# Kernel optimization log

Hardware: AMD Instinct MI355X
Metric: run time of the kernel (lower is better)

The kernel has to match this reference:

```python
import jax, jax.numpy as jnp
import numpy as np

SCALE = 1.0 / np.sqrt(128.0)  # 1/sqrt(head_size)
NEG = -1000000000.0


def setup_inputs() -> dict:
    key = jax.random.key(0)
    k1, k2, k3, k4 = jax.random.split(key, 4)
    B, H, S, D = 2, 16, 2048, 128
    q = jax.random.normal(k1, (B, H, S, D), dtype=jnp.float32)
    k = jax.random.normal(k2, (B, H, S, D), dtype=jnp.float32)
    v = jax.random.normal(k3, (B, H, S, D), dtype=jnp.float32)
    mask = jax.random.randint(k4, (B, S), 0, 2, dtype=jnp.int32)
    return {"q": q, "k": k, "v": v, "mask": mask}


def reference(q, k, v, mask):
    # scores: [B, H, Sq, Sk]
    scores = jnp.einsum("bhqd,bhkd->bhqk", q, k) * SCALE
    m = mask[:, None, None, :]  # [B,1,1,Sk], broadcast over heads and queries
    scores = jnp.where(m == 0, NEG, scores)
    weights = jax.nn.softmax(scores, axis=-1)
    out = jnp.einsum("bhqk,bhkd->bhqd", weights, v)
    return out
```

## Files before the change

### kernel.cpp

```cpp
#include <hip/hip_runtime.h>
#include <hip/hip_bf16.h>

typedef __attribute__((ext_vector_type(8))) short short8;
typedef __attribute__((ext_vector_type(4))) short short4v;
typedef __attribute__((ext_vector_type(4))) float floatx4;

#define NB 2
#define NH 16
#define NBH 32
#define SS 2048
#define DD 128
#define BQ 128
#define BK 32
#define KTILES (SS / BK)
#define KPAIRS (KTILES / 2)
#define SCALE 0.08838834764831845f
#define LOG2E 1.4426950408889634f
#define MAXB 12.0f
#define MASKED_BIAS -100000.0f

#define WC_VM0 0x0F70
#define WC_LGKM0 0xC07F

__device__ __forceinline__ short f2bf(float f) {
  union { float f; unsigned u; } x; x.f = f;
  return (short)((x.u + 0x7FFFu + ((x.u >> 16) & 1u)) >> 16);
}

__device__ __forceinline__ void pack8(short8* dst, float a, float b, float c, float d,
                                      float e, float f, float g, float h) {
  union { __hip_bfloat162 h2[4]; short8 v; } u;
  u.h2[0] = __float22bfloat162_rn(make_float2(a, b));
  u.h2[1] = __float22bfloat162_rn(make_float2(c, d));
  u.h2[2] = __float22bfloat162_rn(make_float2(e, f));
  u.h2[3] = __float22bfloat162_rn(make_float2(g, h));
  *dst = u.v;
}

__device__ __forceinline__ void gload_lds16(const short* g, short* l) {
  __builtin_amdgcn_global_load_lds(
      (const __attribute__((address_space(1))) void*)(g),
      (__attribute__((address_space(3))) void*)(l), 16, 0, 0);
}

__global__ __launch_bounds__(256) void prep_kernel(const float* __restrict__ k,
                                                   const float* __restrict__ v,
                                                   short* __restrict__ kbf,
                                                   short* __restrict__ vtg) {
  __shared__ __align__(16) short Ts[DD * 64];
  const int kb = blockIdx.x, bh = blockIdx.y;
  const int tid = threadIdx.x;
  const size_t base = (size_t)bh * SS * DD + (size_t)(kb * 64) * DD;
  const float* kr = k + base;
  const float* vr = v + base;
  short* kw = kbf + base;

#pragma unroll
  for (int c = 0; c < 8; ++c) {
    int fi = c * 256 + tid;
    float4 a = ((const float4*)kr)[fi];
    short4v o;
    o[0] = f2bf(a.x); o[1] = f2bf(a.y); o[2] = f2bf(a.z); o[3] = f2bf(a.w);
    *(short4v*)(kw + (size_t)fi * 4) = o;
  }

  const int kg = tid & 15;
  const int dg0 = tid >> 4;
#pragma unroll
  for (int c = 0; c < 2; ++c) {
    int dg = dg0 + 16 * c;
    float rr[4][4];
#pragma unroll
    for (int r = 0; r < 4; ++r) {
      float4 a = ((const float4*)vr)[(kg * 4 + r) * 32 + dg];
      rr[r][0] = a.x; rr[r][1] = a.y; rr[r][2] = a.z; rr[r][3] = a.w;
    }
#pragma unroll
    for (int j = 0; j < 4; ++j) {
      int d = dg * 4 + j;
      short4v t;
      t[0] = f2bf(rr[0][j]); t[1] = f2bf(rr[1][j]);
      t[2] = f2bf(rr[2][j]); t[3] = f2bf(rr[3][j]);
      int si = d * 64 + (((kg * 8) ^ ((d & 15) << 3)) >> 1);
      *(short4v*)&Ts[si] = t;
    }
  }
  __syncthreads();

#pragma unroll
  for (int s = 0; s < 4; ++s) {
    int d = s * 32 + (tid >> 3);
    int c = tid & 7, kt2 = c >> 2, g = c & 3;
    int x = (d & 15) << 3;
    short4v lo = *(short4v*)&Ts[d * 64 + ((((kt2 * 8 + g) * 8) ^ x) >> 1)];
    short4v hi = *(short4v*)&Ts[d * 64 + ((((kt2 * 8 + g + 4) * 8) ^ x) >> 1)];
    short8 o;
#pragma unroll
    for (int r = 0; r < 4; ++r) { o[r] = lo[r]; o[4 + r] = hi[r]; }
    *(short8*)(vtg + ((size_t)(bh * DD + d)) * SS + (kb * 2 + kt2) * 32 + g * 8) = o;
  }
}

__global__ __launch_bounds__(256, 2) void fa_kernel(
    const float* __restrict__ q, const short* __restrict__ kbf,
    const short* __restrict__ vtg, const int* __restrict__ mask,
    float* __restrict__ out) {
  __shared__ __align__(16) short Ks[4][BK * DD];
  __shared__ __align__(16) short Vt[4][DD * BK];
  __shared__ float Bias[SS];

  const int tid = threadIdx.x;
  const int wave = tid >> 6;
  const int lane = tid & 63;
  const int l16 = lane & 15;
  const int quad = lane >> 4;

  const int lid = blockIdx.y * 16 + blockIdx.x;
  const int vid = (lid & 7) * 64 + (lid >> 3);
  const int bh = vid >> 4;
  const int q0 = (vid & 15) * BQ;
  const int b = bh >> 4;
  const int poff = ((bh >> 1) & 1) << 4;

  const size_t base = (size_t)bh * SS * DD;
  const float* qg = q + base;
  const short* kg = kbf + base;
  const short* vgb = vtg + (size_t)bh * DD * SS;
  const int* mg = mask + b * SS;
  const float c1 = SCALE * LOG2E, c2 = MAXB * LOG2E;

  short8 qf[2][4];
#pragma unroll
  for (int t = 0; t < 2; ++t) {
    const float* qp = qg + (size_t)(q0 + wave * 32 + t * 16 + l16) * DD;
#pragma unroll
    for (int dc = 0; dc < 4; ++dc) {
      float4 a = *(const float4*)(qp + dc * 32 + quad * 8);
      float4 bb = *(const float4*)(qp + dc * 32 + quad * 8 + 4);
      short8 tt;
      tt[0] = f2bf(a.x); tt[1] = f2bf(a.y); tt[2] = f2bf(a.z); tt[3] = f2bf(a.w);
      tt[4] = f2bf(bb.x); tt[5] = f2bf(bb.y); tt[6] = f2bf(bb.z); tt[7] = f2bf(bb.w);
      qf[t][dc] = tt;
    }
  }

  {
    int i0 = tid * 8;
    int4 m0 = *(const int4*)(mg + i0);
    int4 m1 = *(const int4*)(mg + i0 + 4);
    float4 f0, f1;
    f0.x = m0.x ? -c2 : MASKED_BIAS; f0.y = m0.y ? -c2 : MASKED_BIAS;
    f0.z = m0.z ? -c2 : MASKED_BIAS; f0.w = m0.w ? -c2 : MASKED_BIAS;
    f1.x = m1.x ? -c2 : MASKED_BIAS; f1.y = m1.y ? -c2 : MASKED_BIAS;
    f1.z = m1.z ? -c2 : MASKED_BIAS; f1.w = m1.w ? -c2 : MASKED_BIAS;
    *(float4*)&Bias[i0] = f0;
    *(float4*)&Bias[i0 + 4] = f1;
  }

  floatx4 Oacc[2][8];
#pragma unroll
  for (int t = 0; t < 2; ++t)
#pragma unroll
    for (int f = 0; f < 8; ++f) Oacc[t][f] = (floatx4){0.f, 0.f, 0.f, 0.f};
  float l_acc[2] = {0.f, 0.f};

  const short* kpg[2];
  const short* vpg[2];
  int kls[2], vls[2];
#pragma unroll
  for (int i = 0; i < 2; ++i) {
    int c = wave * 2 + i;
    int krow = c * 4 + (lane >> 4);
    kpg[i] = kg + (size_t)krow * DD + (((lane & 15) ^ (krow & 7)) * 8);
    int d = c * 16 + (lane >> 2);
    vpg[i] = vgb + (size_t)d * SS + (((lane & 3) ^ ((lane >> 3) & 3)) * 8);
    kls[i] = c * 512;
    vls[i] = c * 512;
  }

  int koff[2];
#pragma unroll
  for (int nt = 0; nt < 2; ++nt) koff[nt] = (nt * 16 + l16) * DD;
  const int ksw = l16 & 7;
  const int voff = l16 * 32 + ((quad ^ ((l16 >> 1) & 3)) * 8);

#pragma unroll
  for (int c = 0; c < 2; ++c) {
    const int ktp = 2 * poff + c;
    const size_t kadv = (size_t)ktp * (BK * DD);
    const int vadv = ktp * BK;
#pragma unroll
    for (int i = 0; i < 2; ++i) {
      gload_lds16(kpg[i] + kadv, &Ks[c][kls[i]]);
      gload_lds16(vpg[i] + vadv, &Vt[c][vls[i]]);
    }
  }
  __builtin_amdgcn_s_waitcnt(WC_LGKM0);

#pragma unroll 1
  for (int j = 0; j < KPAIRS; ++j) {
    __builtin_amdgcn_s_waitcnt(WC_VM0);
    __builtin_amdgcn_s_barrier();

    if (j + 1 < KPAIRS) {
      const int pp = (j + 1 + poff) & (KPAIRS - 1);
      const int tb = 2 * ((j + 1) & 1);
#pragma unroll
      for (int c = 0; c < 2; ++c) {
        const int ktn = 2 * pp + c;
        const size_t kadv = (size_t)ktn * (BK * DD);
        const int vadv = ktn * BK;
#pragma unroll
        for (int i = 0; i < 2; ++i) {
          gload_lds16(kpg[i] + kadv, &Ks[tb + c][kls[i]]);
          gload_lds16(vpg[i] + vadv, &Vt[tb + c][vls[i]]);
        }
      }
    }

    const int pp = (j + poff) & (KPAIRS - 1);
    const int ktA = 2 * pp, ktB = ktA + 1;
    const int tbA = 2 * (j & 1), tbB = tbA + 1;
    const short* ksA = &Ks[tbA][0];
    const short* ksB = &Ks[tbB][0];
    const short* vsA = &Vt[tbA][0];
    const short* vsB = &Vt[tbB][0];

    floatx4 sA[2][2], sB[2][2];
#pragma unroll
    for (int t = 0; t < 2; ++t)
#pragma unroll
      for (int nt = 0; nt < 2; ++nt) {
        sA[t][nt] = (floatx4){0.f, 0.f, 0.f, 0.f};
        sB[t][nt] = (floatx4){0.f, 0.f, 0.f, 0.f};
      }
    __builtin_amdgcn_s_setprio(1);
#pragma unroll
    for (int nt = 0; nt < 2; ++nt)
#pragma unroll
      for (int dc = 0; dc < 4; ++dc) {
        short8 kf = *(const short8*)(ksA + koff[nt] + (((dc * 4 + quad) ^ ksw) * 8));
        sA[0][nt] = __builtin_amdgcn_mfma_f32_16x16x32_bf16(kf, qf[0][dc], sA[0][nt], 0, 0, 0);
        sA[1][nt] = __builtin_amdgcn_mfma_f32_16x16x32_bf16(kf, qf[1][dc], sA[1][nt], 0, 0, 0);
      }
#pragma unroll
    for (int nt = 0; nt < 2; ++nt)
#pragma unroll
      for (int dc = 0; dc < 4; ++dc) {
        short8 kf = *(const short8*)(ksB + koff[nt] + (((dc * 4 + quad) ^ ksw) * 8));
        sB[0][nt] = __builtin_amdgcn_mfma_f32_16x16x32_bf16(kf, qf[0][dc], sB[0][nt], 0, 0, 0);
        sB[1][nt] = __builtin_amdgcn_mfma_f32_16x16x32_bf16(kf, qf[1][dc], sB[1][nt], 0, 0, 0);
      }
    __builtin_amdgcn_s_setprio(0);

    float4 bbA0 = *(const float4*)&Bias[ktA * 32 + quad * 4];
    float4 bbA1 = *(const float4*)&Bias[ktA * 32 + 16 + quad * 4];
    short8 pbA[2];
#pragma unroll
    for (int t = 0; t < 2; ++t) {
      float e0 = __builtin_amdgcn_exp2f(fmaf(sA[t][0][0], c1, bbA0.x));
      float e1 = __builtin_amdgcn_exp2f(fmaf(sA[t][0][1], c1, bbA0.y));
      float e2 = __builtin_amdgcn_exp2f(fmaf(sA[t][0][2], c1, bbA0.z));
      float e3 = __builtin_amdgcn_exp2f(fmaf(sA[t][0][3], c1, bbA0.w));
      float g0 = __builtin_amdgcn_exp2f(fmaf(sA[t][1][0], c1, bbA1.x));
      float g1 = __builtin_amdgcn_exp2f(fmaf(sA[t][1][1], c1, bbA1.y));
      float g2 = __builtin_amdgcn_exp2f(fmaf(sA[t][1][2], c1, bbA1.z));
      float g3 = __builtin_amdgcn_exp2f(fmaf(sA[t][1][3], c1, bbA1.w));
      l_acc[t] += ((e0 + e1) + (e2 + e3)) + ((g0 + g1) + (g2 + g3));
      pack8(&pbA[t], e0, e1, e2, e3, g0, g1, g2, g3);
    }

    __builtin_amdgcn_s_setprio(1);
#pragma unroll
    for (int f = 0; f < 8; ++f) {
      short8 vv = *(const short8*)(vsA + f * 512 + voff);
      Oacc[0][f] = __builtin_amdgcn_mfma_f32_16x16x32_bf16(vv, pbA[0], Oacc[0][f], 0, 0, 0);
      Oacc[1][f] = __builtin_amdgcn_mfma_f32_16x16x32_bf16(vv, pbA[1], Oacc[1][f], 0, 0, 0);
    }
    __builtin_amdgcn_s_setprio(0);

    float4 bbB0 = *(const float4*)&Bias[ktB * 32 + quad * 4];
    float4 bbB1 = *(const float4*)&Bias[ktB * 32 + 16 + quad * 4];
    short8 pbB[2];
#pragma unroll
    for (int t = 0; t < 2; ++t) {
      float e0 = __builtin_amdgcn_exp2f(fmaf(sB[t][0][0], c1, bbB0.x));
      float e1 = __builtin_amdgcn_exp2f(fmaf(sB[t][0][1], c1, bbB0.y));
      float e2 = __builtin_amdgcn_exp2f(fmaf(sB[t][0][2], c1, bbB0.z));
      float e3 = __builtin_amdgcn_exp2f(fmaf(sB[t][0][3], c1, bbB0.w));
      float g0 = __builtin_amdgcn_exp2f(fmaf(sB[t][1][0], c1, bbB1.x));
      float g1 = __builtin_amdgcn_exp2f(fmaf(sB[t][1][1], c1, bbB1.y));
      float g2 = __builtin_amdgcn_exp2f(fmaf(sB[t][1][2], c1, bbB1.z));
      float g3 = __builtin_amdgcn_exp2f(fmaf(sB[t][1][3], c1, bbB1.w));
      l_acc[t] += ((e0 + e1) + (e2 + e3)) + ((g0 + g1) + (g2 + g3));
      pack8(&pbB[t], e0, e1, e2, e3, g0, g1, g2, g3);
    }

    __builtin_amdgcn_s_setprio(1);
#pragma unroll
    for (int f = 0; f < 8; ++f) {
      short8 vv = *(const short8*)(vsB + f * 512 + voff);
      Oacc[0][f] = __builtin_amdgcn_mfma_f32_16x16x32_bf16(vv, pbB[0], Oacc[0][f], 0, 0, 0);
      Oacc[1][f] = __builtin_amdgcn_mfma_f32_16x16x32_bf16(vv, pbB[1], Oacc[1][f], 0, 0, 0);
    }
    __builtin_amdgcn_s_setprio(0);
  }

  float* og = out + base;
#pragma unroll
  for (int t = 0; t < 2; ++t) {
    float s = l_acc[t];
    s += __shfl_xor(s, 16);
    s += __shfl_xor(s, 32);
    float inv = 1.0f / s;
    float* orow = og + (size_t)(q0 + wave * 32 + t * 16 + l16) * DD + quad * 4;
#pragma unroll
    for (int f = 0; f < 8; ++f) {
      float4 w;
      w.x = Oacc[t][f][0] * inv;
      w.y = Oacc[t][f][1] * inv;
      w.z = Oacc[t][f][2] * inv;
      w.w = Oacc[t][f][3] * inv;
      *(float4*)(orow + f * 16) = w;
    }
  }
}

extern "C" void kernel_launch(void* const* d_in, const int* in_sizes, int n_in,
                              void* d_out, int out_size, void* d_ws, size_t ws_size,
                              hipStream_t stream) {
  const float* q = (const float*)d_in[0];
  const float* k = (const float*)d_in[1];
  const float* v = (const float*)d_in[2];
  const int* mask = (const int*)d_in[3];
  float* out = (float*)d_out;

  short* kbf = (short*)d_ws;
  short* vtg = kbf + (size_t)NBH * SS * DD;

  prep_kernel<<<dim3(SS / 64, NBH), dim3(256), 0, stream>>>(k, v, kbf, vtg);
  fa_kernel<<<dim3(SS / BQ, NBH), dim3(256), 0, stream>>>(q, kbf, vtg, mask, out);
}
```

Measured before the change: 201.2 us.

## Double query tile per block to 256 rows, four 16-row subtiles per wave

Raises the query block from 128 to 256 rows. Each wave now owns 64 query rows (four 16-row subtiles), so every K/V fragment read from LDS feeds twice as many MFMAs and each block streams K/V for twice as many queries. The grid shrinks to 256 blocks, and launch bounds drop to one block per SIMD to fit the doubled accumulator registers. The rotated K-tile start offset (poff) that spread blocks across the sequence is removed. Occupancy falls to one block per CU with 256 blocks on 256 CUs, which may hurt latency hiding.

```diff
diff --git a/kernel.cpp b/kernel.cpp
--- a/kernel.cpp
+++ b/kernel.cpp
@@ -10,7 +10,7 @@
 #define NBH 32
 #define SS 2048
 #define DD 128
-#define BQ 128
+#define BQ 256
 #define BK 32
 #define KTILES (SS / BK)
 #define KPAIRS (KTILES / 2)
@@ -101,7 +101,7 @@
   }
 }
 
-__global__ __launch_bounds__(256, 2) void fa_kernel(
+__global__ __launch_bounds__(256, 1) void fa_kernel(
     const float* __restrict__ q, const short* __restrict__ kbf,
     const short* __restrict__ vtg, const int* __restrict__ mask,
     float* __restrict__ out) {
@@ -115,12 +115,11 @@
   const int l16 = lane & 15;
   const int quad = lane >> 4;
 
-  const int lid = blockIdx.y * 16 + blockIdx.x;
-  const int vid = (lid & 7) * 64 + (lid >> 3);
-  const int bh = vid >> 4;
-  const int q0 = (vid & 15) * BQ;
+  const int lid = blockIdx.y * 8 + blockIdx.x;
+  const int vid = (lid & 7) * 32 + (lid >> 3);
+  const int bh = vid >> 3;
+  const int q0 = (vid & 7) * BQ;
   const int b = bh >> 4;
-  const int poff = ((bh >> 1) & 1) << 4;
 
   const size_t base = (size_t)bh * SS * DD;
   const float* qg = q + base;
@@ -129,10 +128,10 @@
   const int* mg = mask + b * SS;
   const float c1 = SCALE * LOG2E, c2 = MAXB * LOG2E;
 
-  short8 qf[2][4];
-#pragma unroll
-  for (int t = 0; t < 2; ++t) {
-    const float* qp = qg + (size_t)(q0 + wave * 32 + t * 16 + l16) * DD;
+  short8 qf[4][4];
+#pragma unroll
+  for (int t = 0; t < 4; ++t) {
+    const float* qp = qg + (size_t)(q0 + wave * 64 + t * 16 + l16) * DD;
 #pragma unroll
     for (int dc = 0; dc < 4; ++dc) {
       float4 a = *(const float4*)(qp + dc * 32 + quad * 8);
@@ -157,12 +156,12 @@
     *(float4*)&Bias[i0 + 4] = f1;
   }
 
-  floatx4 Oacc[2][8];
-#pragma unroll
-  for (int t = 0; t < 2; ++t)
+  floatx4 Oacc[4][8];
+#pragma unroll
+  for (int t = 0; t < 4; ++t)
 #pragma unroll
     for (int f = 0; f < 8; ++f) Oacc[t][f] = (floatx4){0.f, 0.f, 0.f, 0.f};
-  float l_acc[2] = {0.f, 0.f};
+  float l_acc[4] = {0.f, 0.f, 0.f, 0.f};
 
   const short* kpg[2];
   const short* vpg[2];
@@ -186,9 +185,8 @@
 
 #pragma unroll
   for (int c = 0; c < 2; ++c) {
-    const int ktp = 2 * poff + c;
-    const size_t kadv = (size_t)ktp * (BK * DD);
-    const int vadv = ktp * BK;
+    const size_t kadv = (size_t)c * (BK * DD);
+    const int vadv = c * BK;
 #pragma unroll
     for (int i = 0; i < 2; ++i) {
       gload_lds16(kpg[i] + kadv, &Ks[c][kls[i]]);
@@ -203,11 +201,10 @@
     __builtin_amdgcn_s_barrier();
 
     if (j + 1 < KPAIRS) {
-      const int pp = (j + 1 + poff) & (KPAIRS - 1);
       const int tb = 2 * ((j + 1) & 1);
 #pragma unroll
       for (int c = 0; c < 2; ++c) {
-        const int ktn = 2 * pp + c;
+        const int ktn = 2 * (j + 1) + c;
         const size_t kadv = (size_t)ktn * (BK * DD);
         const int vadv = ktn * BK;
 #pragma unroll
@@ -218,17 +215,16 @@
       }
     }
 
-    const int pp = (j + poff) & (KPAIRS - 1);
-    const int ktA = 2 * pp, ktB = ktA + 1;
+    const int ktA = 2 * j, ktB = ktA + 1;
     const int tbA = 2 * (j & 1), tbB = tbA + 1;
     const short* ksA = &Ks[tbA][0];
     const short* ksB = &Ks[tbB][0];
     const short* vsA = &Vt[tbA][0];
     const short* vsB = &Vt[tbB][0];
 
-    floatx4 sA[2][2], sB[2][2];
-#pragma unroll
-    for (int t = 0; t < 2; ++t)
+    floatx4 sA[4][2], sB[4][2];
+#pragma unroll
+    for (int t = 0; t < 4; ++t)
 #pragma unroll
       for (int nt = 0; nt < 2; ++nt) {
         sA[t][nt] = (floatx4){0.f, 0.f, 0.f, 0.f};
@@ -240,24 +236,26 @@
 #pragma unroll
       for (int dc = 0; dc < 4; ++dc) {
         short8 kf = *(const short8*)(ksA + koff[nt] + (((dc * 4 + quad) ^ ksw) * 8));
-        sA[0][nt] = __builtin_amdgcn_mfma_f32_16x16x32_bf16(kf, qf[0][dc], sA[0][nt], 0, 0, 0);
-        sA[1][nt] = __builtin_amdgcn_mfma_f32_16x16x32_bf16(kf, qf[1][dc], sA[1][nt], 0, 0, 0);
+#pragma unroll
+        for (int t = 0; t < 4; ++t)
+          sA[t][nt] = __builtin_amdgcn_mfma_f32_16x16x32_bf16(kf, qf[t][dc], sA[t][nt], 0, 0, 0);
       }
 #pragma unroll
     for (int nt = 0; nt < 2; ++nt)
 #pragma unroll
       for (int dc = 0; dc < 4; ++dc) {
         short8 kf = *(const short8*)(ksB + koff[nt] + (((dc * 4 + quad) ^ ksw) * 8));
-        sB[0][nt] = __builtin_amdgcn_mfma_f32_16x16x32_bf16(kf, qf[0][dc], sB[0][nt], 0, 0, 0);
-        sB[1][nt] = __builtin_amdgcn_mfma_f32_16x16x32_bf16(kf, qf[1][dc], sB[1][nt], 0, 0, 0);
+#pragma unroll
+        for (int t = 0; t < 4; ++t)
+          sB[t][nt] = __builtin_amdgcn_mfma_f32_16x16x32_bf16(kf, qf[t][dc], sB[t][nt], 0, 0, 0);
       }
     __builtin_amdgcn_s_setprio(0);
 
     float4 bbA0 = *(const float4*)&Bias[ktA * 32 + quad * 4];
     float4 bbA1 = *(const float4*)&Bias[ktA * 32 + 16 + quad * 4];
-    short8 pbA[2];
-#pragma unroll
-    for (int t = 0; t < 2; ++t) {
+    short8 pbA[4];
+#pragma unroll
+    for (int t = 0; t < 4; ++t) {
       float e0 = __builtin_amdgcn_exp2f(fmaf(sA[t][0][0], c1, bbA0.x));
       float e1 = __builtin_amdgcn_exp2f(fmaf(sA[t][0][1], c1, bbA0.y));
       float e2 = __builtin_amdgcn_exp2f(fmaf(sA[t][0][2], c1, bbA0.z));
@@ -274,16 +272,17 @@
 #pragma unroll
     for (int f = 0; f < 8; ++f) {
       short8 vv = *(const short8*)(vsA + f * 512 + voff);
-      Oacc[0][f] = __builtin_amdgcn_mfma_f32_16x16x32_bf16(vv, pbA[0], Oacc[0][f], 0, 0, 0);
-      Oacc[1][f] = __builtin_amdgcn_mfma_f32_16x16x32_bf16(vv, pbA[1], Oacc[1][f], 0, 0, 0);
+#pragma unroll
+      for (int t = 0; t < 4; ++t)
+        Oacc[t][f] = __builtin_amdgcn_mfma_f32_16x16x32_bf16(vv, pbA[t], Oacc[t][f], 0, 0, 0);
     }
     __builtin_amdgcn_s_setprio(0);
 
     float4 bbB0 = *(const float4*)&Bias[ktB * 32 + quad * 4];
     float4 bbB1 = *(const float4*)&Bias[ktB * 32 + 16 + quad * 4];
-    short8 pbB[2];
-#pragma unroll
-    for (int t = 0; t < 2; ++t) {
+    short8 pbB[4];
+#pragma unroll
+    for (int t = 0; t < 4; ++t) {
       float e0 = __builtin_amdgcn_exp2f(fmaf(sB[t][0][0], c1, bbB0.x));
       float e1 = __builtin_amdgcn_exp2f(fmaf(sB[t][0][1], c1, bbB0.y));
       float e2 = __builtin_amdgcn_exp2f(fmaf(sB[t][0][2], c1, bbB0.z));
@@ -300,20 +299,21 @@
 #pragma unroll
     for (int f = 0; f < 8; ++f) {
       short8 vv = *(const short8*)(vsB + f * 512 + voff);
-      Oacc[0][f] = __builtin_amdgcn_mfma_f32_16x16x32_bf16(vv, pbB[0], Oacc[0][f], 0, 0, 0);
-      Oacc[1][f] = __builtin_amdgcn_mfma_f32_16x16x32_bf16(vv, pbB[1], Oacc[1][f], 0, 0, 0);
+#pragma unroll
+      for (int t = 0; t < 4; ++t)
+        Oacc[t][f] = __builtin_amdgcn_mfma_f32_16x16x32_bf16(vv, pbB[t], Oacc[t][f], 0, 0, 0);
     }
     __builtin_amdgcn_s_setprio(0);
   }
 
   float* og = out + base;
 #pragma unroll
-  for (int t = 0; t < 2; ++t) {
+  for (int t = 0; t < 4; ++t) {
     float s = l_acc[t];
     s += __shfl_xor(s, 16);
     s += __shfl_xor(s, 32);
     float inv = 1.0f / s;
-    float* orow = og + (size_t)(q0 + wave * 32 + t * 16 + l16) * DD + quad * 4;
+    float* orow = og + (size_t)(q0 + wave * 64 + t * 16 + l16) * DD + quad * 4;
 #pragma unroll
     for (int f = 0; f < 8; ++f) {
       float4 w;
```

New measurement: 222.9 us. 1.11x slower.

## Fuse K/V bf16 conversion and V transpose into attention kernel, drop prep pass

Applied to the files above, without the earlier changes.

Removes the separate prep kernel that converted K to bf16 and wrote a transposed bf16 V to workspace. The attention kernel now loads fp32 K/V straight from global memory into registers, converts and transposes them while staging, and writes them into swizzled LDS buffers, with the loads for the next tile pair overlapped with the current tile's MFMA work. This saves a kernel launch and the workspace write/read round trip. In exchange each of the 16 query-block workgroups per head re-reads and re-converts K/V in fp32, roughly doubling global read bytes per block, and staging through registers adds pressure and VALU work.

```diff
diff --git a/kernel.cpp b/kernel.cpp
--- a/kernel.cpp
+++ b/kernel.cpp
@@ -5,8 +5,6 @@
 typedef __attribute__((ext_vector_type(4))) short short4v;
 typedef __attribute__((ext_vector_type(4))) float floatx4;
 
-#define NB 2
-#define NH 16
 #define NBH 32
 #define SS 2048
 #define DD 128
@@ -19,8 +17,9 @@
 #define MAXB 12.0f
 #define MASKED_BIAS -100000.0f
 
-#define WC_VM0 0x0F70
 #define WC_LGKM0 0xC07F
+
+typedef union { float4 v; float f[4]; } f4u;
 
 __device__ __forceinline__ short f2bf(float f) {
   union { float f; unsigned u; } x; x.f = f;
@@ -37,73 +36,9 @@
   *dst = u.v;
 }
 
-__device__ __forceinline__ void gload_lds16(const short* g, short* l) {
-  __builtin_amdgcn_global_load_lds(
-      (const __attribute__((address_space(1))) void*)(g),
-      (__attribute__((address_space(3))) void*)(l), 16, 0, 0);
-}
-
-__global__ __launch_bounds__(256) void prep_kernel(const float* __restrict__ k,
-                                                   const float* __restrict__ v,
-                                                   short* __restrict__ kbf,
-                                                   short* __restrict__ vtg) {
-  __shared__ __align__(16) short Ts[DD * 64];
-  const int kb = blockIdx.x, bh = blockIdx.y;
-  const int tid = threadIdx.x;
-  const size_t base = (size_t)bh * SS * DD + (size_t)(kb * 64) * DD;
-  const float* kr = k + base;
-  const float* vr = v + base;
-  short* kw = kbf + base;
-
-#pragma unroll
-  for (int c = 0; c < 8; ++c) {
-    int fi = c * 256 + tid;
-    float4 a = ((const float4*)kr)[fi];
-    short4v o;
-    o[0] = f2bf(a.x); o[1] = f2bf(a.y); o[2] = f2bf(a.z); o[3] = f2bf(a.w);
-    *(short4v*)(kw + (size_t)fi * 4) = o;
-  }
-
-  const int kg = tid & 15;
-  const int dg0 = tid >> 4;
-#pragma unroll
-  for (int c = 0; c < 2; ++c) {
-    int dg = dg0 + 16 * c;
-    float rr[4][4];
-#pragma unroll
-    for (int r = 0; r < 4; ++r) {
-      float4 a = ((const float4*)vr)[(kg * 4 + r) * 32 + dg];
-      rr[r][0] = a.x; rr[r][1] = a.y; rr[r][2] = a.z; rr[r][3] = a.w;
-    }
-#pragma unroll
-    for (int j = 0; j < 4; ++j) {
-      int d = dg * 4 + j;
-      short4v t;
-      t[0] = f2bf(rr[0][j]); t[1] = f2bf(rr[1][j]);
-      t[2] = f2bf(rr[2][j]); t[3] = f2bf(rr[3][j]);
-      int si = d * 64 + (((kg * 8) ^ ((d & 15) << 3)) >> 1);
-      *(short4v*)&Ts[si] = t;
-    }
-  }
-  __syncthreads();
-
-#pragma unroll
-  for (int s = 0; s < 4; ++s) {
-    int d = s * 32 + (tid >> 3);
-    int c = tid & 7, kt2 = c >> 2, g = c & 3;
-    int x = (d & 15) << 3;
-    short4v lo = *(short4v*)&Ts[d * 64 + ((((kt2 * 8 + g) * 8) ^ x) >> 1)];
-    short4v hi = *(short4v*)&Ts[d * 64 + ((((kt2 * 8 + g + 4) * 8) ^ x) >> 1)];
-    short8 o;
-#pragma unroll
-    for (int r = 0; r < 4; ++r) { o[r] = lo[r]; o[4 + r] = hi[r]; }
-    *(short8*)(vtg + ((size_t)(bh * DD + d)) * SS + (kb * 2 + kt2) * 32 + g * 8) = o;
-  }
-}
-
 __global__ __launch_bounds__(256, 2) void fa_kernel(
-    const float* __restrict__ q, const short* __restrict__ kbf,
-    const short* __restrict__ vtg, const int* __restrict__ mask,
+    const float* __restrict__ q, const float* __restrict__ k,
+    const float* __restrict__ v, const int* __restrict__ mask,
     float* __restrict__ out) {
   __shared__ __align__(16) short Ks[4][BK * DD];
   __shared__ __align__(16) short Vt[4][DD * BK];
@@ -124,10 +59,38 @@
 
   const size_t base = (size_t)bh * SS * DD;
   const float* qg = q + base;
-  const short* kg = kbf + base;
-  const short* vgb = vtg + (size_t)bh * DD * SS;
+  const float* kg = k + base;
+  const float* vg = v + base;
   const int* mg = mask + b * SS;
   const float c1 = SCALE * LOG2E, c2 = MAXB * LOG2E;
+
+  const int krow = wave * 8 + (lane >> 3);
+  const int kswr = krow & 7;
+  const int kc0 = (lane & 7) * 2;
+  const float* kldp = kg + (size_t)krow * DD + (lane & 7) * 16;
+  const int kw0 = krow * DD + ((kc0 ^ kswr) * 8);
+  const int kw1 = krow * DD + (((kc0 + 1) ^ kswr) * 8);
+  const int kg4 = wave * 2 + (lane >> 5);
+  const int dg = lane & 31;
+  const int vgrp = kg4 & 3;
+  const int vhalf = (kg4 >> 2) * 4;
+  const float* vldp = vg + (size_t)(kg4 * 4) * DD + dg * 4;
+
+  f4u kst[2][4], vst[2][4];
+
+  {
+    const int ktA = 2 * poff, ktB = ktA + 1;
+#pragma unroll
+    for (int i = 0; i < 4; ++i) {
+      kst[0][i].v = *(const float4*)(kldp + (size_t)ktA * (BK * DD) + i * 4);
+      kst[1][i].v = *(const float4*)(kldp + (size_t)ktB * (BK * DD) + i * 4);
+    }
+#pragma unroll
+    for (int r = 0; r < 4; ++r) {
+      vst[0][r].v = *(const float4*)(vldp + (size_t)ktA * (BK * DD) + r * DD);
+      vst[1][r].v = *(const float4*)(vldp + (size_t)ktB * (BK * DD) + r * DD);
+    }
+  }
 
   short8 qf[2][4];
 #pragma unroll
@@ -157,26 +120,41 @@
     *(float4*)&Bias[i0 + 4] = f1;
   }
 
+#define WRITE_K(T, BUF)                                                        \
+  {                                                                            \
+    short8 lo_, hi_;                                                           \
+    pack8(&lo_, kst[T][0].f[0], kst[T][0].f[1], kst[T][0].f[2], kst[T][0].f[3],\
+          kst[T][1].f[0], kst[T][1].f[1], kst[T][1].f[2], kst[T][1].f[3]);     \
+    pack8(&hi_, kst[T][2].f[0], kst[T][2].f[1], kst[T][2].f[2], kst[T][2].f[3],\
+          kst[T][3].f[0], kst[T][3].f[1], kst[T][3].f[2], kst[T][3].f[3]);     \
+    *(short8*)&Ks[BUF][kw0] = lo_;                                             \
+    *(short8*)&Ks[BUF][kw1] = hi_;                                             \
+  }
+
+#define WRITE_V(T, BUF)                                                        \
+  {                                                                            \
+    _Pragma("unroll")                                                          \
+    for (int j = 0; j < 4; ++j) {                                              \
+      int d_ = dg * 4 + j;                                                     \
+      int slot_ = ((vgrp ^ ((d_ >> 1) & 3)) * 8) + vhalf;                      \
+      union { __hip_bfloat162 h2[2]; short4v s; } w_;                          \
+      w_.h2[0] = __float22bfloat162_rn(make_float2(vst[T][0].f[j], vst[T][1].f[j])); \
+      w_.h2[1] = __float22bfloat162_rn(make_float2(vst[T][2].f[j], vst[T][3].f[j])); \
+      *(short4v*)&Vt[BUF][d_ * 32 + slot_] = w_.s;                             \
+    }                                                                          \
+  }
+
+  WRITE_K(0, 0) WRITE_K(1, 1)
+  WRITE_V(0, 0) WRITE_V(1, 1)
+  __builtin_amdgcn_s_waitcnt(WC_LGKM0);
+  __builtin_amdgcn_s_barrier();
+
   floatx4 Oacc[2][8];
 #pragma unroll
   for (int t = 0; t < 2; ++t)
 #pragma unroll
     for (int f = 0; f < 8; ++f) Oacc[t][f] = (floatx4){0.f, 0.f, 0.f, 0.f};
   float l_acc[2] = {0.f, 0.f};
-
-  const short* kpg[2];
-  const short* vpg[2];
-  int kls[2], vls[2];
-#pragma unroll
-  for (int i = 0; i < 2; ++i) {
-    int c = wave * 2 + i;
-    int krow = c * 4 + (lane >> 4);
-    kpg[i] = kg + (size_t)krow * DD + (((lane & 15) ^ (krow & 7)) * 8);
-    int d = c * 16 + (lane >> 2);
-    vpg[i] = vgb + (size_t)d * SS + (((lane & 3) ^ ((lane >> 3) & 3)) * 8);
-    kls[i] = c * 512;
-    vls[i] = c * 512;
-  }
 
   int koff[2];
 #pragma unroll
@@ -184,47 +162,27 @@
   const int ksw = l16 & 7;
   const int voff = l16 * 32 + ((quad ^ ((l16 >> 1) & 3)) * 8);
 
-#pragma unroll
-  for (int c = 0; c < 2; ++c) {
-    const int ktp = 2 * poff + c;
-    const size_t kadv = (size_t)ktp * (BK * DD);
-    const int vadv = ktp * BK;
-#pragma unroll
-    for (int i = 0; i < 2; ++i) {
-      gload_lds16(kpg[i] + kadv, &Ks[c][kls[i]]);
-      gload_lds16(vpg[i] + vadv, &Vt[c][vls[i]]);
-    }
-  }
-  __builtin_amdgcn_s_waitcnt(WC_LGKM0);
-
 #pragma unroll 1
   for (int j = 0; j < KPAIRS; ++j) {
-    __builtin_amdgcn_s_waitcnt(WC_VM0);
-    __builtin_amdgcn_s_barrier();
-
-    if (j + 1 < KPAIRS) {
-      const int pp = (j + 1 + poff) & (KPAIRS - 1);
-      const int tb = 2 * ((j + 1) & 1);
-#pragma unroll
-      for (int c = 0; c < 2; ++c) {
-        const int ktn = 2 * pp + c;
-        const size_t kadv = (size_t)ktn * (BK * DD);
-        const int vadv = ktn * BK;
-#pragma unroll
-        for (int i = 0; i < 2; ++i) {
-          gload_lds16(kpg[i] + kadv, &Ks[tb + c][kls[i]]);
-          gload_lds16(vpg[i] + vadv, &Vt[tb + c][vls[i]]);
-        }
-      }
-    }
-
     const int pp = (j + poff) & (KPAIRS - 1);
     const int ktA = 2 * pp, ktB = ktA + 1;
     const int tbA = 2 * (j & 1), tbB = tbA + 1;
+    const int nxA = 2 * ((j + 1) & 1), nxB = nxA + 1;
     const short* ksA = &Ks[tbA][0];
     const short* ksB = &Ks[tbB][0];
     const short* vsA = &Vt[tbA][0];
     const short* vsB = &Vt[tbB][0];
+    const int ppn = (j + 1 + poff) & (KPAIRS - 1);
+    const int ktnA = 2 * ppn, ktnB = ktnA + 1;
+
+    if (j + 1 < KPAIRS) {
+#pragma unroll
+      for (int i = 0; i < 4; ++i) {
+        kst[0][i].v = *(const float4*)(kldp + (size_t)ktnA * (BK * DD) + i * 4);
+        kst[1][i].v = *(const float4*)(kldp + (size_t)ktnB * (BK * DD) + i * 4);
+      }
+      __builtin_amdgcn_sched_barrier(0);
+    }
 
     floatx4 sA[2][2], sB[2][2];
 #pragma unroll
@@ -252,6 +210,16 @@
         sB[1][nt] = __builtin_amdgcn_mfma_f32_16x16x32_bf16(kf, qf[1][dc], sB[1][nt], 0, 0, 0);
       }
     __builtin_amdgcn_s_setprio(0);
+
+    if (j + 1 < KPAIRS) {
+      WRITE_K(0, nxA) WRITE_K(1, nxB)
+#pragma unroll
+      for (int r = 0; r < 4; ++r) {
+        vst[0][r].v = *(const float4*)(vldp + (size_t)ktnA * (BK * DD) + r * DD);
+        vst[1][r].v = *(const float4*)(vldp + (size_t)ktnB * (BK * DD) + r * DD);
+      }
+      __builtin_amdgcn_sched_barrier(0);
+    }
 
     float4 bbA0 = *(const float4*)&Bias[ktA * 32 + quad * 4];
     float4 bbA1 = *(const float4*)&Bias[ktA * 32 + 16 + quad * 4];
@@ -304,7 +272,15 @@
       Oacc[1][f] = __builtin_amdgcn_mfma_f32_16x16x32_bf16(vv, pbB[1], Oacc[1][f], 0, 0, 0);
     }
     __builtin_amdgcn_s_setprio(0);
-  }
+
+    if (j + 1 < KPAIRS) {
+      WRITE_V(0, nxA) WRITE_V(1, nxB)
+      __builtin_amdgcn_s_waitcnt(WC_LGKM0);
+      __builtin_amdgcn_s_barrier();
+    }
+  }
+#undef WRITE_K
+#undef WRITE_V
 
   float* og = out + base;
 #pragma unroll
@@ -335,9 +311,5 @@
   const int* mask = (const int*)d_in[3];
   float* out = (float*)d_out;
 
-  short* kbf = (short*)d_ws;
-  short* vtg = kbf + (size_t)NBH * SS * DD;
-
-  prep_kernel<<<dim3(SS / 64, NBH), dim3(256), 0, stream>>>(k, v, kbf, vtg);
-  fa_kernel<<<dim3(SS / BQ, NBH), dim3(256), 0, stream>>>(q, kbf, vtg, mask, out);
+  fa_kernel<<<dim3(SS / BQ, NBH), dim3(256), 0, stream>>>(q, k, v, mask, out);
 }
```

After: 220.8 us. 1.1x slower.

## Double query tile to 256 rows with 8 waves sharing K/V tiles

Applied to the files above, without the earlier changes.

The query block grows to 256 rows per workgroup with 512 threads (8 waves), so each K/V tile staged in LDS serves twice as many queries and global K/V traffic per query halves. Each wave now issues one K and one V async load per tile instead of two. The per-head staggered key start offset is removed, and waves instead rotate the order of their d-chunk and output-fragment MFMA loops to spread LDS bank access. The trade-off is half as many workgroups (256 on a large CU count) and occupancy limited to one block per CU, which may leave the grid under-filled and reduce latency hiding.

```diff
diff --git a/kernel.cpp b/kernel.cpp
--- a/kernel.cpp
+++ b/kernel.cpp
@@ -10,7 +10,7 @@
 #define NBH 32
 #define SS 2048
 #define DD 128
-#define BQ 128
+#define BQ 256
 #define BK 32
 #define KTILES (SS / BK)
 #define KPAIRS (KTILES / 2)
@@ -101,7 +101,7 @@
   }
 }
 
-__global__ __launch_bounds__(256, 2) void fa_kernel(
+__global__ __launch_bounds__(512, 1) void fa_kernel(
     const float* __restrict__ q, const short* __restrict__ kbf,
     const short* __restrict__ vtg, const int* __restrict__ mask,
     float* __restrict__ out) {
@@ -115,12 +115,11 @@
   const int l16 = lane & 15;
   const int quad = lane >> 4;
 
-  const int lid = blockIdx.y * 16 + blockIdx.x;
-  const int vid = (lid & 7) * 64 + (lid >> 3);
-  const int bh = vid >> 4;
-  const int q0 = (vid & 15) * BQ;
+  const int lid = blockIdx.y * 8 + blockIdx.x;
+  const int vid = (lid & 7) * 32 + (lid >> 3);
+  const int bh = vid >> 3;
+  const int q0 = (vid & 7) * BQ;
   const int b = bh >> 4;
-  const int poff = ((bh >> 1) & 1) << 4;
 
   const size_t base = (size_t)bh * SS * DD;
   const float* qg = q + base;
@@ -145,16 +144,12 @@
   }
 
   {
-    int i0 = tid * 8;
+    int i0 = tid * 4;
     int4 m0 = *(const int4*)(mg + i0);
-    int4 m1 = *(const int4*)(mg + i0 + 4);
-    float4 f0, f1;
+    float4 f0;
     f0.x = m0.x ? -c2 : MASKED_BIAS; f0.y = m0.y ? -c2 : MASKED_BIAS;
     f0.z = m0.z ? -c2 : MASKED_BIAS; f0.w = m0.w ? -c2 : MASKED_BIAS;
-    f1.x = m1.x ? -c2 : MASKED_BIAS; f1.y = m1.y ? -c2 : MASKED_BIAS;
-    f1.z = m1.z ? -c2 : MASKED_BIAS; f1.w = m1.w ? -c2 : MASKED_BIAS;
     *(float4*)&Bias[i0] = f0;
-    *(float4*)&Bias[i0 + 4] = f1;
   }
 
   floatx4 Oacc[2][8];
@@ -164,36 +159,24 @@
     for (int f = 0; f < 8; ++f) Oacc[t][f] = (floatx4){0.f, 0.f, 0.f, 0.f};
   float l_acc[2] = {0.f, 0.f};
 
-  const short* kpg[2];
-  const short* vpg[2];
-  int kls[2], vls[2];
-#pragma unroll
-  for (int i = 0; i < 2; ++i) {
-    int c = wave * 2 + i;
-    int krow = c * 4 + (lane >> 4);
-    kpg[i] = kg + (size_t)krow * DD + (((lane & 15) ^ (krow & 7)) * 8);
-    int d = c * 16 + (lane >> 2);
-    vpg[i] = vgb + (size_t)d * SS + (((lane & 3) ^ ((lane >> 3) & 3)) * 8);
-    kls[i] = c * 512;
-    vls[i] = c * 512;
-  }
+  const int krow = wave * 4 + (lane >> 4);
+  const short* kpg = kg + (size_t)krow * DD + (((lane & 15) ^ (krow & 7)) * 8);
+  const int vd = wave * 16 + (lane >> 2);
+  const short* vpg = vgb + (size_t)vd * SS + (((lane & 3) ^ ((lane >> 3) & 3)) * 8);
+  const int kls = wave * 512;
+  const int vls = wave * 512;
 
   int koff[2];
 #pragma unroll
   for (int nt = 0; nt < 2; ++nt) koff[nt] = (nt * 16 + l16) * DD;
   const int ksw = l16 & 7;
   const int voff = l16 * 32 + ((quad ^ ((l16 >> 1) & 3)) * 8);
+  const int wrot = wave & 3;
 
 #pragma unroll
   for (int c = 0; c < 2; ++c) {
-    const int ktp = 2 * poff + c;
-    const size_t kadv = (size_t)ktp * (BK * DD);
-    const int vadv = ktp * BK;
-#pragma unroll
-    for (int i = 0; i < 2; ++i) {
-      gload_lds16(kpg[i] + kadv, &Ks[c][kls[i]]);
-      gload_lds16(vpg[i] + vadv, &Vt[c][vls[i]]);
-    }
+    gload_lds16(kpg + (size_t)c * (BK * DD), &Ks[c][kls]);
+    gload_lds16(vpg + c * BK, &Vt[c][vls]);
   }
   __builtin_amdgcn_s_waitcnt(WC_LGKM0);
 
@@ -203,23 +186,16 @@
     __builtin_amdgcn_s_barrier();
 
     if (j + 1 < KPAIRS) {
-      const int pp = (j + 1 + poff) & (KPAIRS - 1);
       const int tb = 2 * ((j + 1) & 1);
 #pragma unroll
       for (int c = 0; c < 2; ++c) {
-        const int ktn = 2 * pp + c;
-        const size_t kadv = (size_t)ktn * (BK * DD);
-        const int vadv = ktn * BK;
-#pragma unroll
-        for (int i = 0; i < 2; ++i) {
-          gload_lds16(kpg[i] + kadv, &Ks[tb + c][kls[i]]);
-          gload_lds16(vpg[i] + vadv, &Vt[tb + c][vls[i]]);
-        }
+        const int ktn = 2 * (j + 1) + c;
+        gload_lds16(kpg + (size_t)ktn * (BK * DD), &Ks[tb + c][kls]);
+        gload_lds16(vpg + ktn * BK, &Vt[tb + c][vls]);
       }
     }
 
-    const int pp = (j + poff) & (KPAIRS - 1);
-    const int ktA = 2 * pp, ktB = ktA + 1;
+    const int ktA = 2 * j, ktB = ktA + 1;
     const int tbA = 2 * (j & 1), tbB = tbA + 1;
     const short* ksA = &Ks[tbA][0];
     const short* ksB = &Ks[tbB][0];
@@ -238,7 +214,8 @@
 #pragma unroll
     for (int nt = 0; nt < 2; ++nt)
 #pragma unroll
-      for (int dc = 0; dc < 4; ++dc) {
+      for (int dc0 = 0; dc0 < 4; ++dc0) {
+        const int dc = (dc0 + wrot) & 3;
         short8 kf = *(const short8*)(ksA + koff[nt] + (((dc * 4 + quad) ^ ksw) * 8));
         sA[0][nt] = __builtin_amdgcn_mfma_f32_16x16x32_bf16(kf, qf[0][dc], sA[0][nt], 0, 0, 0);
         sA[1][nt] = __builtin_amdgcn_mfma_f32_16x16x32_bf16(kf, qf[1][dc], sA[1][nt], 0, 0, 0);
@@ -246,7 +223,8 @@
 #pragma unroll
     for (int nt = 0; nt < 2; ++nt)
 #pragma unroll
-      for (int dc = 0; dc < 4; ++dc) {
+      for (int dc0 = 0; dc0 < 4; ++dc0) {
+        const int dc = (dc0 + wrot) & 3;
         short8 kf = *(const short8*)(ksB + koff[nt] + (((dc * 4 + quad) ^ ksw) * 8));
         sB[0][nt] = __builtin_amdgcn_mfma_f32_16x16x32_bf16(kf, qf[0][dc], sB[0][nt], 0, 0, 0);
         sB[1][nt] = __builtin_amdgcn_mfma_f32_16x16x32_bf16(kf, qf[1][dc], sB[1][nt], 0, 0, 0);
@@ -272,7 +250,8 @@
 
     __builtin_amdgcn_s_setprio(1);
 #pragma unroll
-    for (int f = 0; f < 8; ++f) {
+    for (int f0 = 0; f0 < 8; ++f0) {
+      const int f = (f0 + wave) & 7;
       short8 vv = *(const short8*)(vsA + f * 512 + voff);
       Oacc[0][f] = __builtin_amdgcn_mfma_f32_16x16x32_bf16(vv, pbA[0], Oacc[0][f], 0, 0, 0);
       Oacc[1][f] = __builtin_amdgcn_mfma_f32_16x16x32_bf16(vv, pbA[1], Oacc[1][f], 0, 0, 0);
@@ -298,7 +277,8 @@
 
     __builtin_amdgcn_s_setprio(1);
 #pragma unroll
-    for (int f = 0; f < 8; ++f) {
+    for (int f0 = 0; f0 < 8; ++f0) {
+      const int f = (f0 + wave) & 7;
       short8 vv = *(const short8*)(vsB + f * 512 + voff);
       Oacc[0][f] = __builtin_amdgcn_mfma_f32_16x16x32_bf16(vv, pbB[0], Oacc[0][f], 0, 0, 0);
       Oacc[1][f] = __builtin_amdgcn_mfma_f32_16x16x32_bf16(vv, pbB[1], Oacc[1][f], 0, 0, 0);
@@ -339,5 +319,5 @@
   short* vtg = kbf + (size_t)NBH * SS * DD;
 
   prep_kernel<<<dim3(SS / 64, NBH), dim3(256), 0, stream>>>(k, v, kbf, vtg);
-  fa_kernel<<<dim3(SS / BQ, NBH), dim3(256), 0, stream>>>(q, kbf, vtg, mask, out);
-}
+  fa_kernel<<<dim3(SS / BQ, NBH), dim3(512), 0, stream>>>(q, kbf, vtg, mask, out);
+}
```

Result: slower. 687.8 us (+241.9%).
